# Performance work log

Hardware: AMD Instinct MI355X
Metric: run time of the kernel (lower is better)

Reference implementation:

```python
import jax, jax.numpy as jnp
import numpy as np

B, N, P = 8192, 4096, 8
D = N // P  # 512
EPS = 1e-5


def setup_inputs() -> dict:
    key = jax.random.key(0)
    ks = jax.random.split(key, 7)
    bound = 1.0 / np.sqrt(D)
    return {
        "x": jax.random.normal(ks[0], (B, N), dtype=jnp.float32),
        "weights1": jax.random.normal(ks[1], (P, D, D), dtype=jnp.float32) * bound,
        "bias1": jax.random.uniform(ks[2], (N,), jnp.float32, -bound, bound),
        "weights2": jax.random.normal(ks[3], (P, D, D), dtype=jnp.float32) * bound,
        "bias2": jax.random.uniform(ks[4], (N,), jnp.float32, -bound, bound),
        "bn_weight": jnp.ones((N,), jnp.float32),
        "bn_bias": jnp.zeros((N,), jnp.float32),
        "gamma3": jax.random.normal(ks[5], (N,), jnp.float32) * 0.1,
        "beta3": jax.random.normal(ks[6], (N,), jnp.float32) * 0.1,
    }


def _block_matmul(x, w):
    # x: [B, N], w: [P, D, D] -> equivalent to x @ block_diag(*w)
    b = x.shape[0]
    return jnp.einsum("bpd,pde->bpe", x.reshape(b, P, D), w).reshape(b, N)


def reference(x, weights1, bias1, weights2, bias2, bn_weight, bn_bias, gamma3, beta3):
    h = _block_matmul(x, weights1) + bias1  # [B, N]
    # BatchNorm1d in training mode: biased batch statistics over the batch axis
    mean = jnp.mean(h, axis=0)
    var = jnp.mean((h - mean) ** 2, axis=0)
    o1 = (h - mean) * jax.lax.rsqrt(var + EPS) * bn_weight + bn_bias
    o3 = _block_matmul(o1, weights2) + bias2 + x  # residual
    # sigmoid-gated activation: (gamma + sigmoid(beta*x)*(1-gamma)) * x
    o4 = (gamma3 + jax.nn.sigmoid(beta3 * o3) * (1.0 - gamma3)) * o3
    return o4
```

## Files before the change

### kernel.cpp

```cpp
#include <hip/hip_runtime.h>
#include <hip/hip_bf16.h>
#include <cstdint>
#include <cstddef>

#define B_ROWS 8192
#define N_COLS 4096
#define P_BLK 8
#define D_BLK 512
#define EPSV 1e-5f

typedef __bf16 bf16x8 __attribute__((ext_vector_type(8)));
typedef float f32x4 __attribute__((ext_vector_type(4)));

__device__ __forceinline__ void async_ld16(const void* g, void* l) {
    __builtin_amdgcn_global_load_lds(
        (const __attribute__((address_space(1))) void*)g,
        (__attribute__((address_space(3))) void*)l,
        16, 0, 0);
}

__device__ __forceinline__ void decode_tile(int n, int& row_base, int& col_base) {
    const int row_tile = n >> 5;
    const int col_tile = ((n & 7) << 2) | ((n >> 3) & 3);
    row_base = row_tile * 128;
    col_base = col_tile * 128;
}

__global__ __launch_bounds__(256) void prep_k(const float* __restrict__ x,
                                              __hip_bfloat16* __restrict__ xb,
                                              const float* __restrict__ W1,
                                              __hip_bfloat16* __restrict__ w1t) {
    __shared__ float tl[32][33];
    if (blockIdx.x < 16384) {
        size_t i = ((size_t)blockIdx.x * 256 + threadIdx.x) * 8;
        float4 v0 = *(const float4*)(x + i);
        float4 v1 = *(const float4*)(x + i + 4);
        union { __hip_bfloat16 h[8]; uint4 u; } r;
        r.h[0] = __float2bfloat16(v0.x); r.h[1] = __float2bfloat16(v0.y);
        r.h[2] = __float2bfloat16(v0.z); r.h[3] = __float2bfloat16(v0.w);
        r.h[4] = __float2bfloat16(v1.x); r.h[5] = __float2bfloat16(v1.y);
        r.h[6] = __float2bfloat16(v1.z); r.h[7] = __float2bfloat16(v1.w);
        *(uint4*)(xb + i) = r.u;
        return;
    }
    const int n = blockIdx.x - 16384;
    const int p = n >> 8;
    const int rem = n & 255;
    const int d0 = (rem & 15) * 32, e0 = (rem >> 4) * 32;
    const int tx = threadIdx.x & 31, ty = threadIdx.x >> 5;
    const float* Wp = W1 + (size_t)p * D_BLK * D_BLK;
    for (int j = 0; j < 32; j += 8) {
        int d = d0 + ty + j;
        tl[ty + j][tx] = Wp[(size_t)d * D_BLK + e0 + tx];
    }
    __syncthreads();
    __hip_bfloat16* Wtp = w1t + (size_t)p * D_BLK * D_BLK;
    for (int j = 0; j < 32; j += 8) {
        int e = e0 + ty + j;
        Wtp[(size_t)e * D_BLK + d0 + tx] = __float2bfloat16(tl[tx][ty + j]);
    }
}

__global__ __launch_bounds__(256) void mid_k(const float* __restrict__ W2,
                                             const float* __restrict__ sums,
                                             const float* __restrict__ sumsq,
                                             const float* __restrict__ bnw,
                                             const float* __restrict__ bnb,
                                             const float* __restrict__ bias2,
                                             __hip_bfloat16* __restrict__ w2t,
                                             float* __restrict__ b2p) {
    __shared__ float tl[32][33];
    __shared__ float as_[32];
    const float invB = 1.0f / B_ROWS;
    if (blockIdx.x < 2048) {
        const int n = blockIdx.x;
        const int p = n >> 8;
        const int rem = n & 255;
        const int d0 = (rem & 15) * 32, e0 = (rem >> 4) * 32;
        const int tx = threadIdx.x & 31, ty = threadIdx.x >> 5;
        if (threadIdx.x < 32) {
            int idx = p * D_BLK + d0 + threadIdx.x;
            float m = sums[idx] * invB;
            float var = sumsq[idx] * invB - m * m;
            as_[threadIdx.x] = bnw[idx] * rsqrtf(var + EPSV);
        }
        __syncthreads();
        const float* Wp = W2 + (size_t)p * D_BLK * D_BLK;
        for (int j = 0; j < 32; j += 8) {
            int d = d0 + ty + j;
            tl[ty + j][tx] = Wp[(size_t)d * D_BLK + e0 + tx] * as_[ty + j];
        }
        __syncthreads();
        __hip_bfloat16* Wtp = w2t + (size_t)p * D_BLK * D_BLK;
        for (int j = 0; j < 32; j += 8) {
            int e = e0 + ty + j;
            Wtp[(size_t)e * D_BLK + d0 + tx] = __float2bfloat16(tl[tx][ty + j]);
        }
        return;
    }
    const int n2 = blockIdx.x - 2048;
    const int colblk = n2 & 15, chunk = n2 >> 4;
    const int col = colblk * 256 + threadIdx.x;
    const int p = col >> 9;
    const int e = col & (D_BLK - 1);
    const int d0 = chunk * 64;
    float acc = (chunk == 0) ? bias2[col] : 0.0f;
    for (int d = 0; d < 64; d++) {
        int idx = p * D_BLK + d0 + d;
        float m = sums[idx] * invB;
        float var = sumsq[idx] * invB - m * m;
        float ai = bnw[idx] * rsqrtf(var + EPSV);
        float ci = bnb[idx] - m * ai;
        acc += ci * W2[((size_t)p * D_BLK + d0 + d) * D_BLK + e];
    }
    atomicAdd(&b2p[col], acc);
}

__device__ __forceinline__ void gemm_core(const __hip_bfloat16* __restrict__ A,
                                          const __hip_bfloat16* __restrict__ Bt,
                                          int row_base, int col_base,
                                          f32x4 acc[4][4]) {
    __shared__ __hip_bfloat16 As[2][128 * 32];
    __shared__ __hip_bfloat16 Bs[2][128 * 32];

    const int tid = threadIdx.x;
    const int lane = tid & 63;
    const int wave = tid >> 6;
    const int wm = (wave >> 1) * 64;
    const int wn = (wave & 1) * 64;
    const int p = col_base >> 9;
    const int ebase = col_base & (D_BLK - 1);

    const int ar = tid >> 2;
    const int c4 = tid & 3;
    const int kq8 = (c4 ^ ((tid >> 3) & 3)) * 8;
    const int dst_off = ar * 32 + c4 * 8;

    const __hip_bfloat16* a_src0 = A + (size_t)(row_base + ar) * N_COLS + p * D_BLK + kq8;
    const __hip_bfloat16* a_src1 = a_src0 + (size_t)64 * N_COLS;
    const __hip_bfloat16* b_src0 = Bt + (size_t)(p * D_BLK + ebase + ar) * D_BLK + kq8;
    const __hip_bfloat16* b_src1 = b_src0 + (size_t)64 * D_BLK;

    const int fm = lane & 15;
    const int fkoff = ((lane >> 4) ^ ((fm >> 1) & 3)) * 8;

    for (int i = 0; i < 4; i++)
        for (int j = 0; j < 4; j++)
            acc[i][j] = (f32x4){0.0f, 0.0f, 0.0f, 0.0f};

    async_ld16(a_src0, &As[0][dst_off]);
    async_ld16(a_src1, &As[0][dst_off + 64 * 32]);
    async_ld16(b_src0, &Bs[0][dst_off]);
    async_ld16(b_src1, &Bs[0][dst_off + 64 * 32]);

    int cur = 0;
    for (int k0 = 0; k0 < D_BLK; k0 += 32) {
        if (k0 + 32 < D_BLK) {
            __hip_bfloat16* ad = &As[cur ^ 1][dst_off];
            __hip_bfloat16* bd = &Bs[cur ^ 1][dst_off];
            async_ld16(a_src0 + 32, ad);
            async_ld16(a_src1 + 32, ad + 64 * 32);
            async_ld16(b_src0 + 32, bd);
            async_ld16(b_src1 + 32, bd + 64 * 32);
            a_src0 += 32; a_src1 += 32; b_src0 += 32; b_src1 += 32;
            asm volatile("s_waitcnt vmcnt(4)" ::: "memory");
        } else {
            asm volatile("s_waitcnt vmcnt(0)" ::: "memory");
        }
        __builtin_amdgcn_s_barrier();
        asm volatile("" ::: "memory");

        bf16x8 af[4], bfr[4];
        const __hip_bfloat16* Asc = &As[cur][0];
        const __hip_bfloat16* Bsc = &Bs[cur][0];
#pragma unroll
        for (int i = 0; i < 4; i++)
            af[i] = *(const bf16x8*)&Asc[(wm + i * 16 + fm) * 32 + fkoff];
#pragma unroll
        for (int j = 0; j < 4; j++)
            bfr[j] = *(const bf16x8*)&Bsc[(wn + j * 16 + fm) * 32 + fkoff];
        asm volatile("s_waitcnt lgkmcnt(0)" ::: "memory");
        __builtin_amdgcn_sched_barrier(0);
        __builtin_amdgcn_s_barrier();
        asm volatile("" ::: "memory");

#pragma unroll
        for (int i = 0; i < 4; i++)
#pragma unroll
            for (int j = 0; j < 4; j++)
                acc[i][j] = __builtin_amdgcn_mfma_f32_16x16x32_bf16(
                    af[i], bfr[j], acc[i][j], 0, 0, 0);
        cur ^= 1;
    }
}

__global__ __launch_bounds__(256, 4) void gemm1_k(const __hip_bfloat16* __restrict__ xb,
                                                  const __hip_bfloat16* __restrict__ w1t,
                                                  const float* __restrict__ bias1,
                                                  __hip_bfloat16* __restrict__ h,
                                                  float* __restrict__ sum,
                                                  float* __restrict__ sumsq) {
    int row_base, col_base;
    decode_tile(blockIdx.x, row_base, col_base);

    f32x4 acc[4][4];
    gemm_core(xb, w1t, row_base, col_base, acc);

    const int tid = threadIdx.x;
    const int lane = tid & 63;
    const int wave = tid >> 6;
    const int wm = (wave >> 1) * 64;
    const int wn = (wave & 1) * 64;
    const int cr = (lane >> 4) * 4;
    const int cc = lane & 15;

#pragma unroll
    for (int j = 0; j < 4; j++) {
        const int col = col_base + wn + j * 16 + cc;
        const float b1 = bias1[col];
        float s = 0.0f, sq = 0.0f;
#pragma unroll
        for (int i = 0; i < 4; i++) {
            const int row0 = row_base + wm + i * 16 + cr;
#pragma unroll
            for (int r = 0; r < 4; r++) {
                float v = acc[i][j][r] + b1;
                h[(size_t)(row0 + r) * N_COLS + col] = __float2bfloat16(v);
                s += v;
                sq += v * v;
            }
        }
        s  += __shfl_xor(s, 16);  s  += __shfl_xor(s, 32);
        sq += __shfl_xor(sq, 16); sq += __shfl_xor(sq, 32);
        if (lane < 16) {
            atomicAdd(&sum[col], s);
            atomicAdd(&sumsq[col], sq);
        }
    }
}

__global__ __launch_bounds__(256, 4) void gemm2_k(const __hip_bfloat16* __restrict__ h,
                                                  const __hip_bfloat16* __restrict__ w2t,
                                                  const float* __restrict__ bias2p,
                                                  const __hip_bfloat16* __restrict__ xb,
                                                  const float* __restrict__ gamma3,
                                                  const float* __restrict__ beta3,
                                                  float* __restrict__ out) {
    int row_base, col_base;
    decode_tile(blockIdx.x, row_base, col_base);

    f32x4 acc[4][4];
    gemm_core(h, w2t, row_base, col_base, acc);

    const int tid = threadIdx.x;
    const int lane = tid & 63;
    const int wave = tid >> 6;
    const int wm = (wave >> 1) * 64;
    const int wn = (wave & 1) * 64;
    const int cr = (lane >> 4) * 4;
    const int cc = lane & 15;

#pragma unroll
    for (int j = 0; j < 4; j++) {
        const int col = col_base + wn + j * 16 + cc;
        const float bb = bias2p[col];
        const float g  = gamma3[col];
        const float be = beta3[col];
#pragma unroll
        for (int i = 0; i < 4; i++) {
            const int row0 = row_base + wm + i * 16 + cr;
#pragma unroll
            for (int r = 0; r < 4; r++) {
                const size_t idx = (size_t)(row0 + r) * N_COLS + col;
                float o3 = acc[i][j][r] + bb + __bfloat162float(xb[idx]);
                float sg = __fdividef(1.0f, 1.0f + __expf(-be * o3));
                out[idx] = (g + sg * (1.0f - g)) * o3;
            }
        }
    }
}

extern "C" void kernel_launch(void* const* d_in, const int* in_sizes, int n_in,
                              void* d_out, int out_size, void* d_ws, size_t ws_size,
                              hipStream_t stream) {
    const float* x     = (const float*)d_in[0];
    const float* W1    = (const float*)d_in[1];
    const float* bias1 = (const float*)d_in[2];
    const float* W2    = (const float*)d_in[3];
    const float* bias2 = (const float*)d_in[4];
    const float* bnw   = (const float*)d_in[5];
    const float* bnb   = (const float*)d_in[6];
    const float* gam3  = (const float*)d_in[7];
    const float* bet3  = (const float*)d_in[8];
    float* out = (float*)d_out;

    char* ws = (char*)d_ws;
    const size_t XB_BYTES = (size_t)B_ROWS * N_COLS * 2;
    const size_t H_BYTES  = (size_t)B_ROWS * N_COLS * 2;
    const size_t WT_BYTES = (size_t)P_BLK * D_BLK * D_BLK * 2;
    const size_t V_BYTES  = (size_t)N_COLS * 4;

    __hip_bfloat16* xb   = (__hip_bfloat16*)(ws);
    __hip_bfloat16* hbuf = (__hip_bfloat16*)(ws + XB_BYTES);
    __hip_bfloat16* w1t  = (__hip_bfloat16*)(ws + XB_BYTES + H_BYTES);
    __hip_bfloat16* w2t  = (__hip_bfloat16*)(ws + XB_BYTES + H_BYTES + WT_BYTES);
    float* sums  = (float*)(ws + XB_BYTES + H_BYTES + 2 * WT_BYTES);
    float* sumsq = sums + N_COLS;
    float* b2p   = sums + 2 * N_COLS;

    (void)in_sizes; (void)n_in; (void)out_size; (void)ws_size;

    hipMemsetAsync(sums, 0, 3 * V_BYTES, stream);

    prep_k<<<dim3(16384 + 2048), dim3(256), 0, stream>>>(x, xb, W1, w1t);
    gemm1_k<<<dim3((B_ROWS / 128) * (N_COLS / 128)), dim3(256), 0, stream>>>(
        xb, w1t, bias1, hbuf, sums, sumsq);
    mid_k<<<dim3(2048 + 128), dim3(256), 0, stream>>>(
        W2, sums, sumsq, bnw, bnb, bias2, w2t, b2p);
    gemm2_k<<<dim3((B_ROWS / 128) * (N_COLS / 128)), dim3(256), 0, stream>>>(
        hbuf, w2t, b2p, xb, gam3, bet3, out);
}
```

Before: 413.5 us.

## Triple-buffer GEMM LDS tiles and drop second per-iteration barrier

Moves the shared GEMM core from double to triple buffering of the A/B LDS tiles. Loads run two stages ahead, the K loop is fully unrolled, and the second s_barrier per iteration is removed, since the third buffer prevents the next prefetch from overwriting tiles still being read. It also drops the min-blocks-per-CU hint from launch_bounds. The LDS footprint grows by half, which may reduce occupancy, and relaxing the launch bound lets the compiler use more registers.

```diff
diff --git a/kernel.cpp b/kernel.cpp
--- a/kernel.cpp
+++ b/kernel.cpp
@@ -120,8 +120,8 @@
                                           const __hip_bfloat16* __restrict__ Bt,
                                           int row_base, int col_base,
                                           f32x4 acc[4][4]) {
-    __shared__ __hip_bfloat16 As[2][128 * 32];
-    __shared__ __hip_bfloat16 Bs[2][128 * 32];
+    __shared__ __hip_bfloat16 As[3][128 * 32];
+    __shared__ __hip_bfloat16 Bs[3][128 * 32];
 
     const int tid = threadIdx.x;
     const int lane = tid & 63;
@@ -144,25 +144,29 @@
     const int fm = lane & 15;
     const int fkoff = ((lane >> 4) ^ ((fm >> 1) & 3)) * 8;
 
+#pragma unroll
     for (int i = 0; i < 4; i++)
+#pragma unroll
         for (int j = 0; j < 4; j++)
             acc[i][j] = (f32x4){0.0f, 0.0f, 0.0f, 0.0f};
 
-    async_ld16(a_src0, &As[0][dst_off]);
-    async_ld16(a_src1, &As[0][dst_off + 64 * 32]);
-    async_ld16(b_src0, &Bs[0][dst_off]);
-    async_ld16(b_src1, &Bs[0][dst_off + 64 * 32]);
-
-    int cur = 0;
-    for (int k0 = 0; k0 < D_BLK; k0 += 32) {
-        if (k0 + 32 < D_BLK) {
-            __hip_bfloat16* ad = &As[cur ^ 1][dst_off];
-            __hip_bfloat16* bd = &Bs[cur ^ 1][dst_off];
-            async_ld16(a_src0 + 32, ad);
-            async_ld16(a_src1 + 32, ad + 64 * 32);
-            async_ld16(b_src0 + 32, bd);
-            async_ld16(b_src1 + 32, bd + 64 * 32);
-            a_src0 += 32; a_src1 += 32; b_src0 += 32; b_src1 += 32;
+#pragma unroll
+    for (int s = 0; s < 2; s++) {
+        __hip_bfloat16* ad = &As[s][dst_off];
+        __hip_bfloat16* bd = &Bs[s][dst_off];
+        async_ld16(a_src0, ad);
+        async_ld16(a_src1, ad + 64 * 32);
+        async_ld16(b_src0, bd);
+        async_ld16(b_src1, bd + 64 * 32);
+        a_src0 += 32; a_src1 += 32; b_src0 += 32; b_src1 += 32;
+    }
+
+#pragma unroll
+    for (int k = 0; k < 16; ++k) {
+        const int rb = k % 3;
+        const int sb = (k + 2) % 3;
+
+        if (k < 15) {
             asm volatile("s_waitcnt vmcnt(4)" ::: "memory");
         } else {
             asm volatile("s_waitcnt vmcnt(0)" ::: "memory");
@@ -170,9 +174,19 @@
         __builtin_amdgcn_s_barrier();
         asm volatile("" ::: "memory");
 
+        if (k < 14) {
+            __hip_bfloat16* ad = &As[sb][dst_off];
+            __hip_bfloat16* bd = &Bs[sb][dst_off];
+            async_ld16(a_src0, ad);
+            async_ld16(a_src1, ad + 64 * 32);
+            async_ld16(b_src0, bd);
+            async_ld16(b_src1, bd + 64 * 32);
+            a_src0 += 32; a_src1 += 32; b_src0 += 32; b_src1 += 32;
+        }
+
         bf16x8 af[4], bfr[4];
-        const __hip_bfloat16* Asc = &As[cur][0];
-        const __hip_bfloat16* Bsc = &Bs[cur][0];
+        const __hip_bfloat16* Asc = &As[rb][0];
+        const __hip_bfloat16* Bsc = &Bs[rb][0];
 #pragma unroll
         for (int i = 0; i < 4; i++)
             af[i] = *(const bf16x8*)&Asc[(wm + i * 16 + fm) * 32 + fkoff];
@@ -181,8 +195,6 @@
             bfr[j] = *(const bf16x8*)&Bsc[(wn + j * 16 + fm) * 32 + fkoff];
         asm volatile("s_waitcnt lgkmcnt(0)" ::: "memory");
         __builtin_amdgcn_sched_barrier(0);
-        __builtin_amdgcn_s_barrier();
-        asm volatile("" ::: "memory");
 
 #pragma unroll
         for (int i = 0; i < 4; i++)
@@ -190,16 +202,15 @@
             for (int j = 0; j < 4; j++)
                 acc[i][j] = __builtin_amdgcn_mfma_f32_16x16x32_bf16(
                     af[i], bfr[j], acc[i][j], 0, 0, 0);
-        cur ^= 1;
-    }
-}
-
-__global__ __launch_bounds__(256, 4) void gemm1_k(const __hip_bfloat16* __restrict__ xb,
-                                                  const __hip_bfloat16* __restrict__ w1t,
-                                                  const float* __restrict__ bias1,
-                                                  __hip_bfloat16* __restrict__ h,
-                                                  float* __restrict__ sum,
-                                                  float* __restrict__ sumsq) {
+    }
+}
+
+__global__ __launch_bounds__(256) void gemm1_k(const __hip_bfloat16* __restrict__ xb,
+                                               const __hip_bfloat16* __restrict__ w1t,
+                                               const float* __restrict__ bias1,
+                                               __hip_bfloat16* __restrict__ h,
+                                               float* __restrict__ sum,
+                                               float* __restrict__ sumsq) {
     int row_base, col_base;
     decode_tile(blockIdx.x, row_base, col_base);
 
@@ -239,13 +250,13 @@
     }
 }
 
-__global__ __launch_bounds__(256, 4) void gemm2_k(const __hip_bfloat16* __restrict__ h,
-                                                  const __hip_bfloat16* __restrict__ w2t,
-                                                  const float* __restrict__ bias2p,
-                                                  const __hip_bfloat16* __restrict__ xb,
-                                                  const float* __restrict__ gamma3,
-                                                  const float* __restrict__ beta3,
-                                                  float* __restrict__ out) {
+__global__ __launch_bounds__(256) void gemm2_k(const __hip_bfloat16* __restrict__ h,
+                                               const __hip_bfloat16* __restrict__ w2t,
+                                               const float* __restrict__ bias2p,
+                                               const __hip_bfloat16* __restrict__ xb,
+                                               const float* __restrict__ gamma3,
+                                               const float* __restrict__ beta3,
+                                               float* __restrict__ out) {
     int row_base, col_base;
     decode_tile(blockIdx.x, row_base, col_base);
 
```

After: 404.0 us. 1.02x faster.

## Fuse fp32-to-bf16 conversion of x into first GEMM's A-tile loading

Applied to the files above, without the earlier changes.

The separate prep pass that converted x to bf16 is removed. gemm1 now loads fp32 x directly, converts it in registers, writes it to shared memory, and has one column tile per block group store the bf16 copy for the residual in gemm2. The W1 transpose becomes its own small kernel, and launch_bounds occupancy hints are dropped from both GEMMs. This saves a full read and write of x, but every GEMM1 block now reads fp32 A, twice the bytes, four times across column tiles, and the conversion work sits inside the main loop, which may raise register pressure.

```diff
diff --git a/kernel.cpp b/kernel.cpp
--- a/kernel.cpp
+++ b/kernel.cpp
@@ -26,38 +26,31 @@
     col_base = col_tile * 128;
 }
 
-__global__ __launch_bounds__(256) void prep_k(const float* __restrict__ x,
-                                              __hip_bfloat16* __restrict__ xb,
-                                              const float* __restrict__ W1,
-                                              __hip_bfloat16* __restrict__ w1t) {
-    __shared__ float tl[32][33];
-    if (blockIdx.x < 16384) {
-        size_t i = ((size_t)blockIdx.x * 256 + threadIdx.x) * 8;
-        float4 v0 = *(const float4*)(x + i);
-        float4 v1 = *(const float4*)(x + i + 4);
-        union { __hip_bfloat16 h[8]; uint4 u; } r;
-        r.h[0] = __float2bfloat16(v0.x); r.h[1] = __float2bfloat16(v0.y);
-        r.h[2] = __float2bfloat16(v0.z); r.h[3] = __float2bfloat16(v0.w);
-        r.h[4] = __float2bfloat16(v1.x); r.h[5] = __float2bfloat16(v1.y);
-        r.h[6] = __float2bfloat16(v1.z); r.h[7] = __float2bfloat16(v1.w);
-        *(uint4*)(xb + i) = r.u;
-        return;
-    }
-    const int n = blockIdx.x - 16384;
-    const int p = n >> 8;
-    const int rem = n & 255;
-    const int d0 = (rem & 15) * 32, e0 = (rem >> 4) * 32;
-    const int tx = threadIdx.x & 31, ty = threadIdx.x >> 5;
-    const float* Wp = W1 + (size_t)p * D_BLK * D_BLK;
+__device__ __forceinline__ uint4 cvt8(float4 a, float4 b) {
+    union { __hip_bfloat16 hx[8]; uint4 u; } r;
+    r.hx[0] = __float2bfloat16(a.x); r.hx[1] = __float2bfloat16(a.y);
+    r.hx[2] = __float2bfloat16(a.z); r.hx[3] = __float2bfloat16(a.w);
+    r.hx[4] = __float2bfloat16(b.x); r.hx[5] = __float2bfloat16(b.y);
+    r.hx[6] = __float2bfloat16(b.z); r.hx[7] = __float2bfloat16(b.w);
+    return r.u;
+}
+
+__global__ __launch_bounds__(256) void tr_w_k(const float* __restrict__ W,
+                                              __hip_bfloat16* __restrict__ Wt) {
+    __shared__ float t[32][33];
+    int p = blockIdx.z;
+    int d0 = blockIdx.x * 32, e0 = blockIdx.y * 32;
+    const float* Wp = W + (size_t)p * D_BLK * D_BLK;
     for (int j = 0; j < 32; j += 8) {
-        int d = d0 + ty + j;
-        tl[ty + j][tx] = Wp[(size_t)d * D_BLK + e0 + tx];
+        int d = d0 + threadIdx.y + j;
+        t[threadIdx.y + j][threadIdx.x] = Wp[(size_t)d * D_BLK + e0 + threadIdx.x];
     }
     __syncthreads();
-    __hip_bfloat16* Wtp = w1t + (size_t)p * D_BLK * D_BLK;
+    __hip_bfloat16* Wtp = Wt + (size_t)p * D_BLK * D_BLK;
     for (int j = 0; j < 32; j += 8) {
-        int e = e0 + ty + j;
-        Wtp[(size_t)e * D_BLK + d0 + tx] = __float2bfloat16(tl[tx][ty + j]);
+        int e = e0 + threadIdx.y + j;
+        Wtp[(size_t)e * D_BLK + d0 + threadIdx.x] =
+            __float2bfloat16(t[threadIdx.x][threadIdx.y + j]);
     }
 }
 
@@ -194,26 +187,116 @@
     }
 }
 
-__global__ __launch_bounds__(256, 4) void gemm1_k(const __hip_bfloat16* __restrict__ xb,
-                                                  const __hip_bfloat16* __restrict__ w1t,
-                                                  const float* __restrict__ bias1,
-                                                  __hip_bfloat16* __restrict__ h,
-                                                  float* __restrict__ sum,
-                                                  float* __restrict__ sumsq) {
+__global__ __launch_bounds__(256) void gemm1_k(const float* __restrict__ x,
+                                               const __hip_bfloat16* __restrict__ w1t,
+                                               const float* __restrict__ bias1,
+                                               __hip_bfloat16* __restrict__ xb,
+                                               __hip_bfloat16* __restrict__ h,
+                                               float* __restrict__ sum,
+                                               float* __restrict__ sumsq) {
+    __shared__ __hip_bfloat16 As[2][128 * 32];
+    __shared__ __hip_bfloat16 Bs[2][128 * 32];
+
     int row_base, col_base;
     decode_tile(blockIdx.x, row_base, col_base);
-
-    f32x4 acc[4][4];
-    gemm_core(xb, w1t, row_base, col_base, acc);
 
     const int tid = threadIdx.x;
     const int lane = tid & 63;
     const int wave = tid >> 6;
     const int wm = (wave >> 1) * 64;
     const int wn = (wave & 1) * 64;
+    const int p = col_base >> 9;
+    const int ebase = col_base & (D_BLK - 1);
+
+    const int ar = tid >> 2;
+    const int c4 = tid & 3;
+    const int kq8 = (c4 ^ ((tid >> 3) & 3)) * 8;
+    const int dst_off = ar * 32 + c4 * 8;
+    const bool do_store = ((col_base >> 7) & 3) == 0;
+
+    const float* ax0 = x + (size_t)(row_base + ar) * N_COLS + p * D_BLK + kq8;
+    const float* ax1 = ax0 + (size_t)64 * N_COLS;
+    const __hip_bfloat16* b_src0 = w1t + (size_t)(p * D_BLK + ebase + ar) * D_BLK + kq8;
+    const __hip_bfloat16* b_src1 = b_src0 + (size_t)64 * D_BLK;
+    __hip_bfloat16* xs0 = xb + (size_t)(row_base + ar) * N_COLS + p * D_BLK + kq8;
+    __hip_bfloat16* xs1 = xs0 + (size_t)64 * N_COLS;
+
+    const int fm = lane & 15;
+    const int fkoff = ((lane >> 4) ^ ((fm >> 1) & 3)) * 8;
+
+    f32x4 acc[4][4];
+#pragma unroll
+    for (int i = 0; i < 4; i++)
+#pragma unroll
+        for (int j = 0; j < 4; j++)
+            acc[i][j] = (f32x4){0.0f, 0.0f, 0.0f, 0.0f};
+
+    {
+        float4 a0a = *(const float4*)ax0, a0b = *(const float4*)(ax0 + 4);
+        float4 a1a = *(const float4*)ax1, a1b = *(const float4*)(ax1 + 4);
+        async_ld16(b_src0, &Bs[0][dst_off]);
+        async_ld16(b_src1, &Bs[0][dst_off + 64 * 32]);
+        ax0 += 32; ax1 += 32; b_src0 += 32; b_src1 += 32;
+        uint4 r0 = cvt8(a0a, a0b);
+        uint4 r1 = cvt8(a1a, a1b);
+        *(uint4*)&As[0][dst_off] = r0;
+        *(uint4*)&As[0][dst_off + 64 * 32] = r1;
+        if (do_store) { *(uint4*)xs0 = r0; *(uint4*)xs1 = r1; xs0 += 32; xs1 += 32; }
+        asm volatile("s_waitcnt lgkmcnt(0)" ::: "memory");
+    }
+
+    int cur = 0;
+#pragma unroll 2
+    for (int k = 0; k < 16; ++k) {
+        float4 na0a, na0b, na1a, na1b;
+        if (k < 15) {
+            na0a = *(const float4*)ax0; na0b = *(const float4*)(ax0 + 4);
+            na1a = *(const float4*)ax1; na1b = *(const float4*)(ax1 + 4);
+            __hip_bfloat16* bd = &Bs[cur ^ 1][dst_off];
+            async_ld16(b_src0, bd);
+            async_ld16(b_src1, bd + 64 * 32);
+            ax0 += 32; ax1 += 32; b_src0 += 32; b_src1 += 32;
+            asm volatile("s_waitcnt vmcnt(6)" ::: "memory");
+        } else {
+            asm volatile("s_waitcnt vmcnt(0)" ::: "memory");
+        }
+        __builtin_amdgcn_s_barrier();
+        asm volatile("" ::: "memory");
+
+        bf16x8 af[4], bfr[4];
+        const __hip_bfloat16* Asc = &As[cur][0];
+        const __hip_bfloat16* Bsc = &Bs[cur][0];
+#pragma unroll
+        for (int i = 0; i < 4; i++)
+            af[i] = *(const bf16x8*)&Asc[(wm + i * 16 + fm) * 32 + fkoff];
+#pragma unroll
+        for (int j = 0; j < 4; j++)
+            bfr[j] = *(const bf16x8*)&Bsc[(wn + j * 16 + fm) * 32 + fkoff];
+        asm volatile("s_waitcnt lgkmcnt(0)" ::: "memory");
+        __builtin_amdgcn_sched_barrier(0);
+        __builtin_amdgcn_s_barrier();
+        asm volatile("" ::: "memory");
+
+#pragma unroll
+        for (int i = 0; i < 4; i++)
+#pragma unroll
+            for (int j = 0; j < 4; j++)
+                acc[i][j] = __builtin_amdgcn_mfma_f32_16x16x32_bf16(
+                    af[i], bfr[j], acc[i][j], 0, 0, 0);
+
+        if (k < 15) {
+            uint4 r0 = cvt8(na0a, na0b);
+            uint4 r1 = cvt8(na1a, na1b);
+            *(uint4*)&As[cur ^ 1][dst_off] = r0;
+            *(uint4*)&As[cur ^ 1][dst_off + 64 * 32] = r1;
+            if (do_store) { *(uint4*)xs0 = r0; *(uint4*)xs1 = r1; xs0 += 32; xs1 += 32; }
+            asm volatile("s_waitcnt lgkmcnt(0)" ::: "memory");
+        }
+        cur ^= 1;
+    }
+
     const int cr = (lane >> 4) * 4;
     const int cc = lane & 15;
-
 #pragma unroll
     for (int j = 0; j < 4; j++) {
         const int col = col_base + wn + j * 16 + cc;
@@ -239,13 +322,13 @@
     }
 }
 
-__global__ __launch_bounds__(256, 4) void gemm2_k(const __hip_bfloat16* __restrict__ h,
-                                                  const __hip_bfloat16* __restrict__ w2t,
-                                                  const float* __restrict__ bias2p,
-                                                  const __hip_bfloat16* __restrict__ xb,
-                                                  const float* __restrict__ gamma3,
-                                                  const float* __restrict__ beta3,
-                                                  float* __restrict__ out) {
+__global__ __launch_bounds__(256) void gemm2_k(const __hip_bfloat16* __restrict__ h,
+                                               const __hip_bfloat16* __restrict__ w2t,
+                                               const float* __restrict__ bias2p,
+                                               const __hip_bfloat16* __restrict__ xb,
+                                               const float* __restrict__ gamma3,
+                                               const float* __restrict__ beta3,
+                                               float* __restrict__ out) {
     int row_base, col_base;
     decode_tile(blockIdx.x, row_base, col_base);
 
@@ -312,9 +395,9 @@
 
     hipMemsetAsync(sums, 0, 3 * V_BYTES, stream);
 
-    prep_k<<<dim3(16384 + 2048), dim3(256), 0, stream>>>(x, xb, W1, w1t);
+    tr_w_k<<<dim3(16, 16, 8), dim3(32, 8), 0, stream>>>(W1, w1t);
     gemm1_k<<<dim3((B_ROWS / 128) * (N_COLS / 128)), dim3(256), 0, stream>>>(
-        xb, w1t, bias1, hbuf, sums, sumsq);
+        x, w1t, bias1, xb, hbuf, sums, sumsq);
     mid_k<<<dim3(2048 + 128), dim3(256), 0, stream>>>(
         W2, sums, sumsq, bnw, bnb, bias2, w2t, b2p);
     gemm2_k<<<dim3((B_ROWS / 128) * (N_COLS / 128)), dim3(256), 0, stream>>>(
```

Measured after the change: 425.3 us. 2.8% more time.
